# Performance work log

Hardware: AMD Instinct MI355X
Metric: run time of the kernel (lower is better)

The kernel has to match this reference:

```python
import jax, jax.numpy as jnp
import numpy as np

N_SERIES = 1024  # N; x carries 3N stacked time-synchronous nodes
GCN_DEPTH = 2
IN_DIM = 64
H_DIM = 64


def setup_inputs() -> dict:
    key = jax.random.key(0)
    k = jax.random.split(key, 6)
    B, C, N3 = 64, IN_DIM, 3 * N_SERIES
    x = jax.random.normal(k[0], (N3, B, C), dtype=jnp.float32)
    A = jax.random.normal(k[1], (N3, N3), dtype=jnp.float32) * 0.02
    # Linear2d (1x1 conv) params per depth; act='glu' -> out = 2*h_dim
    s0 = 1.0 / np.sqrt(IN_DIM)
    s1 = 1.0 / np.sqrt(H_DIM)
    W0 = jax.random.uniform(k[2], (2 * H_DIM, IN_DIM), jnp.float32, -s0, s0)
    b0 = jax.random.uniform(k[3], (2 * H_DIM,), jnp.float32, -s0, s0)
    W1 = jax.random.uniform(k[4], (2 * H_DIM, H_DIM), jnp.float32, -s1, s1)
    b1 = jax.random.uniform(k[5], (2 * H_DIM,), jnp.float32, -s1, s1)
    return {"x": x, "A": A, "W0": W0, "b0": b0, "W1": W1, "b1": b1}


def reference(x, A, W0, b0, W1, b1):
    # x: (3N, B, C) -> (B, C, 3N)
    h = jnp.transpose(x, (1, 2, 0))
    convs = []
    for W, b in ((W0, b0), (W1, b1)):
        # GCN2d flow='tgt_to_src': h[b,c,v] = sum_w h[b,c,w] * A[v,w]  (L=1 squeezed)
        g = jnp.einsum('bcw,vw->bcv', h, A)
        # Linear2d 1x1 conv: channels C -> 2*h_dim, then GLU gate
        y = jnp.einsum('oc,bcv->bov', W, g) + b[None, :, None]
        lhs, rhs = jnp.split(y, 2, axis=1)
        h = lhs * jax.nn.sigmoid(rhs)          # (B, h_dim, 3N)
        convs.append(jnp.transpose(h, (2, 0, 1)))  # (3N, B, h_dim)
    # crop the middle N nodes of each depth, then max over depth
    cropped = jnp.stack([c[N_SERIES:2 * N_SERIES] for c in convs], axis=0)
    return jnp.max(cropped, axis=0)  # (N, B, h_dim)
```

## Files before the change

kernel.cpp:

```cpp
#include <hip/hip_runtime.h>
#include <hip/hip_bf16.h>
#include <stdint.h>

typedef __attribute__((ext_vector_type(8))) short s16x8;
typedef __attribute__((ext_vector_type(4))) float f32x4;
typedef __attribute__((ext_vector_type(8))) unsigned short u16x8;
typedef __attribute__((ext_vector_type(4))) unsigned short u16x4;

__device__ __forceinline__ float bf2f(unsigned short u) {
  union { uint32_t u; float f; } v; v.u = ((uint32_t)u) << 16; return v.f;
}
__device__ __forceinline__ unsigned short f2bf(float f) {
  union { float f; uint32_t u; } v; v.f = f;
  uint32_t u = v.u;
  return (unsigned short)((u + 0x7fffu + ((u >> 16) & 1u)) >> 16);
}
__device__ __forceinline__ void load_lds16(const void* g, void* l) {
  __builtin_amdgcn_global_load_lds(
      (const __attribute__((address_space(1))) void*)g,
      (__attribute__((address_space(3))) void*)l, 16, 0, 0);
}

template <int N>
__device__ __forceinline__ void vmw() {
  if constexpr (N == 0) asm volatile("s_waitcnt vmcnt(0)" ::: "memory");
  else if constexpr (N == 1) asm volatile("s_waitcnt vmcnt(1)" ::: "memory");
  else if constexpr (N == 2) asm volatile("s_waitcnt vmcnt(2)" ::: "memory");
  else if constexpr (N == 3) asm volatile("s_waitcnt vmcnt(3)" ::: "memory");
  else if constexpr (N == 4) asm volatile("s_waitcnt vmcnt(4)" ::: "memory");
  else if constexpr (N == 5) asm volatile("s_waitcnt vmcnt(5)" ::: "memory");
  else if constexpr (N == 6) asm volatile("s_waitcnt vmcnt(6)" ::: "memory");
  else if constexpr (N == 7) asm volatile("s_waitcnt vmcnt(7)" ::: "memory");
  else asm volatile("s_waitcnt vmcnt(8)" ::: "memory");
}
#define SBAR() asm volatile("s_barrier" ::: "memory")


__global__ __launch_bounds__(256) void k_prep(const void* __restrict__ xin,
                                              const void* __restrict__ Ain,
                                              const void* __restrict__ W0,
                                              const void* __restrict__ b0,
                                              const void* __restrict__ W1,
                                              const void* __restrict__ b1,
                                              unsigned short* __restrict__ xtp,
                                              unsigned short* __restrict__ Abp,
                                              unsigned short* __restrict__ wb) {
  __shared__ __align__(16) unsigned short sh[64 * 65];
  const int t = threadIdx.x;
  const int bid = blockIdx.x;
  int fp;
  {
    uint32_t u = ((const uint32_t*)xin)[(t & 63) * 97 + 1];
    int e = (u >> 7) & 0xFF;
    unsigned long long m = __ballot(e > 150);
    fp = (__popcll(m) > 6) ? 1 : 0;
  }

  if (bid < 3072) {
    const int w0 = (bid % 48) * 64;
    const int m0 = (bid / 48) * 64;
    if (fp) {
      const float* xf = (const float*)xin;
#pragma unroll
      for (int rep = 0; rep < 4; ++rep) {
        int vi = t + rep * 256;
        int r = vi >> 4;
        int c4 = (vi & 15) * 4;
        f32x4 v = *(const f32x4*)(xf + (uint64_t)(w0 + r) * 4096 + m0 + c4);
#pragma unroll
        for (int u = 0; u < 4; ++u) sh[(c4 + u) * 65 + r] = f2bf(v[u]);
      }
    } else {
      const unsigned short* xb = (const unsigned short*)xin;
#pragma unroll
      for (int rep = 0; rep < 2; ++rep) {
        int vi = t + rep * 256;
        int r = vi >> 3;
        int c8 = (vi & 7) * 8;
        u16x8 v = *(const u16x8*)(xb + (uint64_t)(w0 + r) * 4096 + m0 + c8);
#pragma unroll
        for (int u = 0; u < 8; ++u) sh[(c8 + u) * 65 + r] = v[u];
      }
    }
    __syncthreads();
    unsigned short* dst = xtp + ((uint64_t)(m0 >> 6) * 48 + (w0 >> 6)) * 4096;
#pragma unroll
    for (int rep = 0; rep < 2; ++rep) {
      int vi = t + rep * 256;
      int kb = vi >> 6, r = vi & 63;
      u16x8 v;
#pragma unroll
      for (int u = 0; u < 8; ++u) v[u] = sh[r * 65 + kb * 8 + u];
      *(u16x8*)(dst + kb * 512 + r * 8) = v;
    }
  } else if (bid < 5376) {
    const int b2 = bid - 3072;
    const int kt = b2 % 48, rt = b2 / 48;
    if (fp) {
      const float* Af = (const float*)Ain;
#pragma unroll
      for (int rep = 0; rep < 4; ++rep) {
        int vi = t + rep * 256;
        int r = vi >> 4;
        int c4 = (vi & 15) * 4;
        f32x4 v = *(const f32x4*)(Af + (uint64_t)(rt * 64 + r) * 3072 + kt * 64 + c4);
        int kb = c4 >> 3, e = c4 & 7;
#pragma unroll
        for (int u = 0; u < 4; ++u) sh[kb * 520 + r * 8 + e + u] = f2bf(v[u]);
      }
    } else {
      const unsigned short* Ab16 = (const unsigned short*)Ain;
#pragma unroll
      for (int rep = 0; rep < 2; ++rep) {
        int vi = t + rep * 256;
        int r = vi >> 3;
        int c8 = (vi & 7) * 8;
        u16x8 v = *(const u16x8*)(Ab16 + (uint64_t)(rt * 64 + r) * 3072 + kt * 64 + c8);
#pragma unroll
        for (int u = 0; u < 8; ++u) sh[(c8 >> 3) * 520 + r * 8 + u] = v[u];
      }
    }
    __syncthreads();
    unsigned short* dst = Abp + ((uint64_t)rt * 48 + kt) * 4096;
#pragma unroll
    for (int rep = 0; rep < 2; ++rep) {
      int vi = t + rep * 256;
      int kb = vi >> 6, r = vi & 63;
      u16x8 v;
#pragma unroll
      for (int u = 0; u < 8; ++u) v[u] = sh[kb * 520 + r * 8 + u];
      *(u16x8*)(dst + kb * 512 + r * 8) = v;
    }
  } else {
    for (int i = t; i < 16640; i += 256) {
      const void* src; int off;
      if (i < 8192)        { src = W0; off = i; }
      else if (i < 8320)   { src = b0; off = i - 8192; }
      else if (i < 16512)  { src = W1; off = i - 8320; }
      else                 { src = b1; off = i - 16512; }
      wb[i] = fp ? f2bf(((const float*)src)[off]) : ((const unsigned short*)src)[off];
    }
  }
}

template <int BM, int KTOT, bool FUSEMAX>
__global__ __launch_bounds__(512, 2) void k_gemm_glu5(
    const unsigned short* __restrict__ Am,
    const unsigned short* __restrict__ Bm,
    const unsigned short* __restrict__ W,
    const unsigned short* __restrict__ bias,
    unsigned short* __restrict__ H,
    const unsigned short* __restrict__ Hprev,
    float* __restrict__ outp,
    int Vtot) {
  constexpr int BN  = 256;
  constexpr int IF  = BM / 32;
  constexpr int NPH = (IF > 4) ? 2 : 1;
  constexpr int IPH = IF / NPH;
  constexpr int APL = (BM / 64) * 4;
  constexpr int P   = APL + 16;
  constexpr int QF  = P / 8;
  constexpr int QR  = P - QF * 8;
  constexpr int PPW = QF + (QR ? 1 : 0);
  constexpr int BUFS = P * 512;
  constexpr int NT  = KTOT / 32;
  constexpr int Kt  = KTOT / 64;
  constexpr int NRB = BM / 16;
  constexpr int EPL = BM * 264;
  constexpr int SME = (4 * BUFS > EPL) ? 4 * BUFS : EPL;

  __shared__ __align__(16) unsigned short smem[SME];

  const int t    = threadIdx.x;
  const int lane = t & 63;
  const int wid  = t >> 6;
  const int wV   = wid >> 2;
  const int wM   = wid & 3;
  const int fr   = lane & 15;
  const int q4   = lane >> 4;
  const int v0   = blockIdx.x * BM;
  const int m0   = blockIdx.y * BN;
  const int art0 = v0 >> 6;
  const int brt0 = m0 >> 6;

  const int myq = QF + ((QR && wid < QR) ? 1 : 0);
  const unsigned short* srcb[PPW];
  int ldso[PPW];
#pragma unroll
  for (int q = 0; q < PPW; ++q) {
    int pi = wid + 8 * q;
    if (pi >= P) pi = P - 1;
    const int isA = pi < APL;
    const int rtl = (isA ? pi : pi - APL) >> 2;
    const int pb  = pi & 3;
    const unsigned short* base =
        isA ? (Am + (uint64_t)(art0 + rtl) * Kt * 4096)
            : (Bm + (uint64_t)(brt0 + rtl) * Kt * 4096);
    srcb[q] = base + pb * 512 + lane * 8;
    ldso[q] = pi * 512;
  }

  int aoff[IF], boff[4];
#pragma unroll
  for (int i = 0; i < IF; ++i) {
    const int row = wV * (BM / 2) + i * 16 + fr;
    aoff[i] = ((row >> 6) * 4 + q4) * 512 + (row & 63) * 8;
  }
#pragma unroll
  for (int j = 0; j < 4; ++j)
    boff[j] = (APL + wM * 4 + q4) * 512 + (j * 16 + fr) * 8;

  f32x4 acc[IF][4] = {};

#pragma unroll
  for (int pt = 0; pt < 3; ++pt)
#pragma unroll
    for (int q = 0; q < PPW; ++q)
      if (q < myq)
        load_lds16(srcb[q] + pt * 2048, smem + pt * BUFS + ldso[q]);
  if (QR && wid < QR) { vmw<2 * (QF + 1)>(); } else { vmw<2 * QF>(); }
  SBAR();

#pragma unroll 4
  for (int tt = 0; tt < NT; ++tt) {
    const unsigned short* buf = smem + (tt & 3) * BUFS;
    s16x8 bfr[4];
#pragma unroll
    for (int ph = 0; ph < NPH; ++ph) {
      if (ph == 0) {
#pragma unroll
        for (int j = 0; j < 4; ++j)
          bfr[j] = *(const s16x8*)(buf + boff[j]);
      }
      s16x8 afr[IPH];
#pragma unroll
      for (int ii = 0; ii < IPH; ++ii)
        afr[ii] = *(const s16x8*)(buf + aoff[ph * IPH + ii]);
      if (tt + 3 < NT) {
        unsigned short* dst = smem + ((tt + 3) & 3) * BUFS;
#pragma unroll
        for (int q = 0; q < PPW; ++q)
          if ((q % NPH) == ph && q < myq)
            load_lds16(srcb[q] + (uint64_t)(tt + 3) * 2048, dst + ldso[q]);
      }
      SBAR();
      __builtin_amdgcn_s_setprio(1);
#pragma unroll
      for (int ii = 0; ii < IPH; ++ii)
#pragma unroll
        for (int j = 0; j < 4; ++j)
          acc[ph * IPH + ii][j] = __builtin_amdgcn_mfma_f32_16x16x32_bf16(
              afr[ii], bfr[j], acc[ph * IPH + ii][j], 0, 0, 0);
      __builtin_amdgcn_s_setprio(0);
      if (ph == NPH - 1) {
        if (tt + 3 < NT) {
          if (QR && wid < QR) { vmw<2 * (QF + 1)>(); } else { vmw<2 * QF>(); }
        } else if (tt + 2 < NT) {
          if (QR && wid < QR) { vmw<QF + 1>(); } else { vmw<QF>(); }
        } else {
          vmw<0>();
        }
      }
      SBAR();
    }
  }

  __syncthreads();
  {
    const int rr = q4 * 4;
#pragma unroll
    for (int i = 0; i < IF; ++i)
#pragma unroll
      for (int j = 0; j < 4; ++j) {
        const int col = wM * 64 + j * 16 + fr;
#pragma unroll
        for (int r = 0; r < 4; ++r) {
          const int row = wV * (BM / 2) + i * 16 + rr + r;
          smem[row * 264 + col] = f2bf(acc[i][j][r]);
        }
      }
  }
  __syncthreads();

  s16x8 wf[2][8];
#pragma unroll
  for (int ksi = 0; ksi < 2; ++ksi)
#pragma unroll
    for (int j = 0; j < 8; ++j)
      wf[ksi][j] = *(const s16x8*)(W + (j * 16 + fr) * 64 + ksi * 32 + q4 * 8);
  float bj[8];
#pragma unroll
  for (int j = 0; j < 8; ++j) bj[j] = bf2f(bias[j * 16 + fr]);

  const int Vt = Vtot >> 6;
#pragma unroll
  for (int rep = 0; rep < (NRB + 7) / 8; ++rep) {
    const int rb = rep * 8 + wid;
    if (rb < NRB) {
#pragma unroll
      for (int bb = 0; bb < 4; ++bb) {
        f32x4 acc2[8] = {};
#pragma unroll
        for (int ksi = 0; ksi < 2; ++ksi) {
          s16x8 af = *(const s16x8*)(smem + (rb * 16 + fr) * 264 + bb * 64 +
                                     ksi * 32 + q4 * 8);
#pragma unroll
          for (int j = 0; j < 8; ++j)
            acc2[j] = __builtin_amdgcn_mfma_f32_16x16x32_bf16(af, wf[ksi][j],
                                                              acc2[j], 0, 0, 0);
        }
        const int v = v0 + rb * 16 + q4 * 4;
#pragma unroll
        for (int j = 0; j < 4; ++j) {
          const int o = j * 16 + fr;
          const int hrow = m0 + bb * 64 + o;
          if constexpr (FUSEMAX) {
            const int c = 1024 + v;
            u16x4 hv = *(const u16x4*)(Hprev +
                ((uint64_t)(hrow >> 6) * 48 + (c >> 6)) * 4096 +
                ((c >> 3) & 7) * 512 + (hrow & 63) * 8 + (c & 7));
            float* op = outp + (uint64_t)v * 4096 + hrow;
#pragma unroll
            for (int r = 0; r < 4; ++r) {
              float lhs = acc2[j][r] + bj[j];
              float rhs = acc2[j + 4][r] + bj[j + 4];
              float sg = 1.0f / (1.0f + __expf(-rhs));
              op[(uint64_t)r * 4096] = fmaxf(lhs * sg, bf2f(hv[r]));
            }
          } else {
            u16x4 pk;
#pragma unroll
            for (int r = 0; r < 4; ++r) {
              float lhs = acc2[j][r] + bj[j];
              float rhs = acc2[j + 4][r] + bj[j + 4];
              float sg = 1.0f / (1.0f + __expf(-rhs));
              pk[r] = f2bf(lhs * sg);
            }
            *(u16x4*)(H + ((uint64_t)(hrow >> 6) * Vt + (v >> 6)) * 4096 +
                      ((v >> 3) & 7) * 512 + (hrow & 63) * 8 + (v & 7)) = pk;
          }
        }
      }
    }
  }
}

extern "C" void kernel_launch(void* const* d_in, const int* in_sizes, int n_in,
                              void* d_out, int out_size, void* d_ws, size_t ws_size,
                              hipStream_t stream) {
  (void)in_sizes; (void)n_in; (void)out_size; (void)ws_size;
  const void* x  = d_in[0];
  const void* A  = d_in[1];
  const void* W0 = d_in[2];
  const void* b0 = d_in[3];
  const void* W1 = d_in[4];
  const void* b1 = d_in[5];
  float* out = (float*)d_out;

  char* ws = (char*)d_ws;
  unsigned short* Xtp = (unsigned short*)(ws + 0);
  unsigned short* Abp = (unsigned short*)(ws + 25165824);
  unsigned short* Wb  = (unsigned short*)(ws + 44040192);
  unsigned short* H1p = (unsigned short*)(ws + 44105728);

  k_prep<<<5377, 256, 0, stream>>>(x, A, W0, b0, W1, b1, Xtp, Abp, Wb);
  k_gemm_glu5<192, 3072, false><<<dim3(16, 16), 512, 0, stream>>>(
      Abp, Xtp, Wb, Wb + 8192, H1p, nullptr, nullptr, 3072);
  k_gemm_glu5<64, 3072, true><<<dim3(16, 16), 512, 0, stream>>>(
      Abp + (uint64_t)16 * 48 * 4096, H1p, Wb + 8320, Wb + 16512,
      nullptr, H1p, out, 1024);
}
```

Before: 268.2 us.

## Split second-layer GEMM over K with fp32 partials and separate GLU finish kernel

Measured after the change: 269.1 us. About the same (+0.3%).

```diff
diff --git a/kernel.cpp b/kernel.cpp
--- a/kernel.cpp
+++ b/kernel.cpp
@@ -34,6 +34,10 @@
   else asm volatile("s_waitcnt vmcnt(8)" ::: "memory");
 }
 #define SBAR() asm volatile("s_barrier" ::: "memory")
+
+__device__ __forceinline__ int sigma(int rt) {
+  return rt < 16 ? rt : (rt < 32 ? rt + 16 : rt - 16);
+}
 
 
 __global__ __launch_bounds__(256) void k_prep(const void* __restrict__ xin,
@@ -121,7 +125,7 @@
       }
     }
     __syncthreads();
-    unsigned short* dst = Abp + ((uint64_t)rt * 48 + kt) * 4096;
+    unsigned short* dst = Abp + ((uint64_t)sigma(rt) * 48 + kt) * 4096;
 #pragma unroll
     for (int rep = 0; rep < 2; ++rep) {
       int vi = t + rep * 256;
@@ -143,17 +147,17 @@
   }
 }
 
-template <int BM, int KTOT, bool FUSEMAX>
-__global__ __launch_bounds__(512, 2) void k_gemm_glu5(
+template <int BM, int MODE>
+__global__ __launch_bounds__(512, 2) void k_gemm_glu6(
     const unsigned short* __restrict__ Am,
     const unsigned short* __restrict__ Bm,
     const unsigned short* __restrict__ W,
     const unsigned short* __restrict__ bias,
     unsigned short* __restrict__ H,
-    const unsigned short* __restrict__ Hprev,
-    float* __restrict__ outp,
+    float* __restrict__ Pout0,
+    float* __restrict__ Pout1,
     int Vtot) {
-  constexpr int BN  = 256;
+  constexpr int KT64 = 48;
   constexpr int IF  = BM / 32;
   constexpr int NPH = (IF > 4) ? 2 : 1;
   constexpr int IPH = IF / NPH;
@@ -163,11 +167,10 @@
   constexpr int QR  = P - QF * 8;
   constexpr int PPW = QF + (QR ? 1 : 0);
   constexpr int BUFS = P * 512;
-  constexpr int NT  = KTOT / 32;
-  constexpr int Kt  = KTOT / 64;
   constexpr int NRB = BM / 16;
   constexpr int EPL = BM * 264;
-  constexpr int SME = (4 * BUFS > EPL) ? 4 * BUFS : EPL;
+  constexpr int SME = (MODE == 1) ? 4 * BUFS
+                                  : ((4 * BUFS > EPL) ? 4 * BUFS : EPL);
 
   __shared__ __align__(16) unsigned short smem[SME];
 
@@ -178,10 +181,19 @@
   const int wM   = wid & 3;
   const int fr   = lane & 15;
   const int q4   = lane >> 4;
-  const int v0   = blockIdx.x * BM;
-  const int m0   = blockIdx.y * BN;
-  const int art0 = v0 >> 6;
+  const int m0   = blockIdx.y * 256;
   const int brt0 = m0 >> 6;
+
+  int v0, kt0, ntk, artB;
+  if constexpr (MODE == 1) {
+    v0   = (blockIdx.x >> 1) * BM;
+    kt0  = (blockIdx.x & 1) * 48;
+    ntk  = 48;
+    artB = 16;
+  } else {
+    v0 = blockIdx.x * BM; kt0 = 0; ntk = 96; artB = 0;
+  }
+  const int art0 = artB + (v0 >> 6);
 
   const int myq = QF + ((QR && wid < QR) ? 1 : 0);
   const unsigned short* srcb[PPW];
@@ -194,8 +206,8 @@
     const int rtl = (isA ? pi : pi - APL) >> 2;
     const int pb  = pi & 3;
     const unsigned short* base =
-        isA ? (Am + (uint64_t)(art0 + rtl) * Kt * 4096)
-            : (Bm + (uint64_t)(brt0 + rtl) * Kt * 4096);
+        isA ? (Am + (uint64_t)sigma(art0 + rtl) * KT64 * 4096)
+            : (Bm + (uint64_t)(brt0 + rtl) * KT64 * 4096);
     srcb[q] = base + pb * 512 + lane * 8;
     ldso[q] = pi * 512;
   }
@@ -217,12 +229,12 @@
 #pragma unroll
     for (int q = 0; q < PPW; ++q)
       if (q < myq)
-        load_lds16(srcb[q] + pt * 2048, smem + pt * BUFS + ldso[q]);
+        load_lds16(srcb[q] + (uint64_t)(kt0 + pt) * 2048, smem + pt * BUFS + ldso[q]);
   if (QR && wid < QR) { vmw<2 * (QF + 1)>(); } else { vmw<2 * QF>(); }
   SBAR();
 
 #pragma unroll 4
-  for (int tt = 0; tt < NT; ++tt) {
+  for (int tt = 0; tt < ntk; ++tt) {
     const unsigned short* buf = smem + (tt & 3) * BUFS;
     s16x8 bfr[4];
 #pragma unroll
@@ -236,12 +248,12 @@
 #pragma unroll
       for (int ii = 0; ii < IPH; ++ii)
         afr[ii] = *(const s16x8*)(buf + aoff[ph * IPH + ii]);
-      if (tt + 3 < NT) {
+      if (tt + 3 < ntk) {
         unsigned short* dst = smem + ((tt + 3) & 3) * BUFS;
 #pragma unroll
         for (int q = 0; q < PPW; ++q)
           if ((q % NPH) == ph && q < myq)
-            load_lds16(srcb[q] + (uint64_t)(tt + 3) * 2048, dst + ldso[q]);
+            load_lds16(srcb[q] + (uint64_t)(kt0 + tt + 3) * 2048, dst + ldso[q]);
       }
       SBAR();
       __builtin_amdgcn_s_setprio(1);
@@ -253,9 +265,9 @@
               afr[ii], bfr[j], acc[ph * IPH + ii][j], 0, 0, 0);
       __builtin_amdgcn_s_setprio(0);
       if (ph == NPH - 1) {
-        if (tt + 3 < NT) {
+        if (tt + 3 < ntk) {
           if (QR && wid < QR) { vmw<2 * (QF + 1)>(); } else { vmw<2 * QF>(); }
-        } else if (tt + 2 < NT) {
+        } else if (tt + 2 < ntk) {
           if (QR && wid < QR) { vmw<QF + 1>(); } else { vmw<QF>(); }
         } else {
           vmw<0>();
@@ -265,9 +277,8 @@
     }
   }
 
-  __syncthreads();
-  {
-    const int rr = q4 * 4;
+  if constexpr (MODE == 1) {
+    float* Pout = (blockIdx.x & 1) ? Pout1 : Pout0;
 #pragma unroll
     for (int i = 0; i < IF; ++i)
 #pragma unroll
@@ -275,59 +286,59 @@
         const int col = wM * 64 + j * 16 + fr;
 #pragma unroll
         for (int r = 0; r < 4; ++r) {
-          const int row = wV * (BM / 2) + i * 16 + rr + r;
-          smem[row * 264 + col] = f2bf(acc[i][j][r]);
+          const int row = wV * (BM / 2) + i * 16 + q4 * 4 + r;
+          Pout[(uint64_t)(v0 + row) * 4096 + m0 + col] = acc[i][j][r];
         }
       }
-  }
-  __syncthreads();
-
-  s16x8 wf[2][8];
-#pragma unroll
-  for (int ksi = 0; ksi < 2; ++ksi)
-#pragma unroll
-    for (int j = 0; j < 8; ++j)
-      wf[ksi][j] = *(const s16x8*)(W + (j * 16 + fr) * 64 + ksi * 32 + q4 * 8);
-  float bj[8];
-#pragma unroll
-  for (int j = 0; j < 8; ++j) bj[j] = bf2f(bias[j * 16 + fr]);
-
-  const int Vt = Vtot >> 6;
-#pragma unroll
-  for (int rep = 0; rep < (NRB + 7) / 8; ++rep) {
-    const int rb = rep * 8 + wid;
-    if (rb < NRB) {
-#pragma unroll
-      for (int bb = 0; bb < 4; ++bb) {
-        f32x4 acc2[8] = {};
-#pragma unroll
-        for (int ksi = 0; ksi < 2; ++ksi) {
-          s16x8 af = *(const s16x8*)(smem + (rb * 16 + fr) * 264 + bb * 64 +
-                                     ksi * 32 + q4 * 8);
-#pragma unroll
-          for (int j = 0; j < 8; ++j)
-            acc2[j] = __builtin_amdgcn_mfma_f32_16x16x32_bf16(af, wf[ksi][j],
-                                                              acc2[j], 0, 0, 0);
+    return;
+  } else {
+    __syncthreads();
+    {
+      const int rr = q4 * 4;
+#pragma unroll
+      for (int i = 0; i < IF; ++i)
+#pragma unroll
+        for (int j = 0; j < 4; ++j) {
+          const int col = wM * 64 + j * 16 + fr;
+#pragma unroll
+          for (int r = 0; r < 4; ++r) {
+            const int row = wV * (BM / 2) + i * 16 + rr + r;
+            smem[row * 264 + col] = f2bf(acc[i][j][r]);
+          }
         }
-        const int v = v0 + rb * 16 + q4 * 4;
-#pragma unroll
-        for (int j = 0; j < 4; ++j) {
-          const int o = j * 16 + fr;
-          const int hrow = m0 + bb * 64 + o;
-          if constexpr (FUSEMAX) {
-            const int c = 1024 + v;
-            u16x4 hv = *(const u16x4*)(Hprev +
-                ((uint64_t)(hrow >> 6) * 48 + (c >> 6)) * 4096 +
-                ((c >> 3) & 7) * 512 + (hrow & 63) * 8 + (c & 7));
-            float* op = outp + (uint64_t)v * 4096 + hrow;
-#pragma unroll
-            for (int r = 0; r < 4; ++r) {
-              float lhs = acc2[j][r] + bj[j];
-              float rhs = acc2[j + 4][r] + bj[j + 4];
-              float sg = 1.0f / (1.0f + __expf(-rhs));
-              op[(uint64_t)r * 4096] = fmaxf(lhs * sg, bf2f(hv[r]));
-            }
-          } else {
+    }
+    __syncthreads();
+
+    s16x8 wf[2][8];
+#pragma unroll
+    for (int ksi = 0; ksi < 2; ++ksi)
+#pragma unroll
+      for (int j = 0; j < 8; ++j)
+        wf[ksi][j] = *(const s16x8*)(W + (j * 16 + fr) * 64 + ksi * 32 + q4 * 8);
+    float bj[8];
+#pragma unroll
+    for (int j = 0; j < 8; ++j) bj[j] = bf2f(bias[j * 16 + fr]);
+
+    const int Vt = Vtot >> 6;
+#pragma unroll
+    for (int rep = 0; rep < (NRB + 7) / 8; ++rep) {
+      const int rb = rep * 8 + wid;
+      if (rb < NRB) {
+#pragma unroll
+        for (int bb = 0; bb < 4; ++bb) {
+          f32x4 acc2[8] = {};
+#pragma unroll
+          for (int ksi = 0; ksi < 2; ++ksi) {
+            s16x8 af = *(const s16x8*)(smem + (rb * 16 + fr) * 264 + bb * 64 +
+                                       ksi * 32 + q4 * 8);
+#pragma unroll
+            for (int j = 0; j < 8; ++j)
+              acc2[j] = __builtin_amdgcn_mfma_f32_16x16x32_bf16(af, wf[ksi][j],
+                                                                acc2[j], 0, 0, 0);
+          }
+          const int v = v0 + rb * 16 + q4 * 4;
+#pragma unroll
+          for (int j = 0; j < 4; ++j) {
             u16x4 pk;
 #pragma unroll
             for (int r = 0; r < 4; ++r) {
@@ -336,10 +347,85 @@
               float sg = 1.0f / (1.0f + __expf(-rhs));
               pk[r] = f2bf(lhs * sg);
             }
+            const int o = j * 16 + fr;
+            const int hrow = m0 + bb * 64 + o;
             *(u16x4*)(H + ((uint64_t)(hrow >> 6) * Vt + (v >> 6)) * 4096 +
                       ((v >> 3) & 7) * 512 + (hrow & 63) * 8 + (v & 7)) = pk;
           }
         }
+      }
+    }
+  }
+}
+
+__global__ __launch_bounds__(512) void k_glufin(const float* __restrict__ P0f,
+                                                const float* __restrict__ P1f,
+                                                const unsigned short* __restrict__ W,
+                                                const unsigned short* __restrict__ bias,
+                                                const unsigned short* __restrict__ Hprev,
+                                                float* __restrict__ outp) {
+  __shared__ __align__(16) unsigned short g[64 * 264];
+  const int t    = threadIdx.x;
+  const int lane = t & 63;
+  const int wid  = t >> 6;
+  const int fr   = lane & 15;
+  const int q4   = lane >> 4;
+  const int v0   = blockIdx.x * 64;
+  const int m0   = blockIdx.y * 256;
+
+#pragma unroll
+  for (int rep = 0; rep < 8; ++rep) {
+    int vi = t + rep * 512;
+    int row = vi >> 6;
+    int c4 = (vi & 63) * 4;
+    uint64_t idx = (uint64_t)(v0 + row) * 4096 + m0 + c4;
+    f32x4 a = *(const f32x4*)(P0f + idx);
+    f32x4 b = *(const f32x4*)(P1f + idx);
+#pragma unroll
+    for (int u = 0; u < 4; ++u) g[row * 264 + c4 + u] = f2bf(a[u] + b[u]);
+  }
+  __syncthreads();
+
+  s16x8 wf[2][8];
+#pragma unroll
+  for (int ksi = 0; ksi < 2; ++ksi)
+#pragma unroll
+    for (int j = 0; j < 8; ++j)
+      wf[ksi][j] = *(const s16x8*)(W + (j * 16 + fr) * 64 + ksi * 32 + q4 * 8);
+  float bj[8];
+#pragma unroll
+  for (int j = 0; j < 8; ++j) bj[j] = bf2f(bias[j * 16 + fr]);
+
+  const int rb = wid & 3;
+#pragma unroll
+  for (int bb2 = 0; bb2 < 2; ++bb2) {
+    const int bb = (wid >> 2) * 2 + bb2;
+    f32x4 acc2[8] = {};
+#pragma unroll
+    for (int ksi = 0; ksi < 2; ++ksi) {
+      s16x8 af = *(const s16x8*)(g + (rb * 16 + fr) * 264 + bb * 64 +
+                                 ksi * 32 + q4 * 8);
+#pragma unroll
+      for (int j = 0; j < 8; ++j)
+        acc2[j] = __builtin_amdgcn_mfma_f32_16x16x32_bf16(af, wf[ksi][j],
+                                                          acc2[j], 0, 0, 0);
+    }
+    const int v = v0 + rb * 16 + q4 * 4;
+#pragma unroll
+    for (int j = 0; j < 4; ++j) {
+      const int o = j * 16 + fr;
+      const int hrow = m0 + bb * 64 + o;
+      const int c = 1024 + v;
+      u16x4 hv = *(const u16x4*)(Hprev +
+          ((uint64_t)(hrow >> 6) * 48 + (c >> 6)) * 4096 +
+          ((c >> 3) & 7) * 512 + (hrow & 63) * 8 + (c & 7));
+      float* op = outp + (uint64_t)v * 4096 + hrow;
+#pragma unroll
+      for (int r = 0; r < 4; ++r) {
+        float lhs = acc2[j][r] + bj[j];
+        float rhs = acc2[j + 4][r] + bj[j + 4];
+        float sg = 1.0f / (1.0f + __expf(-rhs));
+        op[(uint64_t)r * 4096] = fmaxf(lhs * sg, bf2f(hv[r]));
       }
     }
   }
@@ -362,11 +448,14 @@
   unsigned short* Abp = (unsigned short*)(ws + 25165824);
   unsigned short* Wb  = (unsigned short*)(ws + 44040192);
   unsigned short* H1p = (unsigned short*)(ws + 44105728);
+  float* Pk0 = (float*)(ws + 0);
+  float* Pk1 = (float*)(ws + 16777216);
 
   k_prep<<<5377, 256, 0, stream>>>(x, A, W0, b0, W1, b1, Xtp, Abp, Wb);
-  k_gemm_glu5<192, 3072, false><<<dim3(16, 16), 512, 0, stream>>>(
+  k_gemm_glu6<192, 0><<<dim3(16, 16), 512, 0, stream>>>(
       Abp, Xtp, Wb, Wb + 8192, H1p, nullptr, nullptr, 3072);
-  k_gemm_glu5<64, 3072, true><<<dim3(16, 16), 512, 0, stream>>>(
-      Abp + (uint64_t)16 * 48 * 4096, H1p, Wb + 8320, Wb + 16512,
-      nullptr, H1p, out, 1024);
-}
+  k_gemm_glu6<128, 1><<<dim3(16, 16), 512, 0, stream>>>(
+      Abp, H1p, nullptr, nullptr, nullptr, Pk0, Pk1, 1024);
+  k_glufin<<<dim3(16, 16), 512, 0, stream>>>(Pk0, Pk1, Wb + 8320, Wb + 16512,
+                                             H1p, out);
+}
```
